# Kernel tuning notes

Hardware: AMD Instinct MI355X
Metric: run time of the kernel (lower is better)

## Reference

```python
import jax, jax.numpy as jnp
import numpy as np

N_NODES = 50000
N_EDGES = 800000
D_IN = 512
D_OUT = 256


def setup_inputs() -> dict:
    key = jax.random.key(0)
    k1, k2, k3 = jax.random.split(key, 3)
    x = jax.random.normal(k1, (N_NODES, D_IN), dtype=jnp.float32)
    edge_index = jax.random.randint(k2, (2, N_EDGES), 0, N_NODES, dtype=jnp.int64)
    # Glorot-style init for the GCN weight, zero bias (PyG defaults)
    W = jax.random.normal(k3, (D_IN, D_OUT), dtype=jnp.float32) * (1.0 / np.sqrt(D_IN))
    b = jnp.zeros((D_OUT,), dtype=jnp.float32)
    return {"x": x, "edge_index": edge_index, "W": W, "b": b}


def reference(x, edge_index, W, b):
    N = x.shape[0]
    # 1) dense linear transform (the compute-heavy GEMM)
    xw = x @ W  # [N, d_out]

    # 2) add self-loops (PyG GCNConv default)
    loop = jnp.arange(N, dtype=edge_index.dtype)
    row = jnp.concatenate([edge_index[0], loop])  # sources
    col = jnp.concatenate([edge_index[1], loop])  # targets

    # 3) symmetric normalization deg^{-1/2} on targets (in-degree incl. self-loops)
    deg = jax.ops.segment_sum(jnp.ones_like(col, dtype=xw.dtype), col, num_segments=N)
    dinv = jnp.where(deg > 0, jax.lax.rsqrt(deg), 0.0)
    norm = dinv[row] * dinv[col]  # [E+N]

    # 4) gather source features, scale, scatter-add to targets
    msgs = xw[row] * norm[:, None]  # [E+N, d_out]
    agg = jax.ops.segment_sum(msgs, col, num_segments=N)  # [N, d_out]

    # 5) bias + ReLU (dropout is identity in eval mode)
    return jax.nn.relu(agg + b)
```

## Files before the change

### kernel.cpp

```cpp
#include <hip/hip_runtime.h>
#include <hip/hip_bf16.h>

#define N_NODES 50000
#define N_EDGES 800000
#define D_IN    512
#define D_OUT   256
#define NBLK_SCAN ((N_NODES + 1023) / 1024)
#define GEMM_NWG (((N_NODES + 127) / 128) * 2)
#define GEMM_Q   (GEMM_NWG / 8)
#define GEMM_R   (GEMM_NWG % 8)

typedef short s8v  __attribute__((ext_vector_type(8)));
typedef float f32x4 __attribute__((ext_vector_type(4)));

__device__ __forceinline__ unsigned short bf16b(float f) {
    __hip_bfloat16 h = __float2bfloat16(f);
    return *reinterpret_cast<unsigned short*>(&h);
}
__device__ __forceinline__ float bflo(unsigned u) { return __uint_as_float(u << 16); }
__device__ __forceinline__ float bfhi(unsigned u) { return __uint_as_float(u & 0xffff0000u); }

#define GLD16(gp, lp)                                                           \
    __builtin_amdgcn_global_load_lds(                                           \
        (const __attribute__((address_space(1))) unsigned int*)(const void*)(gp),\
        (__attribute__((address_space(3))) unsigned int*)(void*)(lp), 16, 0, 0)

__device__ __forceinline__ int wave_incl_scan(int v, int lane) {
    #pragma unroll
    for (int d = 1; d < 64; d <<= 1) {
        int u = __shfl_up(v, d, 64);
        if (lane >= d) v += u;
    }
    return v;
}


__global__ void k_count(const int* __restrict__ col, int* __restrict__ cnt) {
    int i = (blockIdx.x * 256 + threadIdx.x) * 2;
    if (i < N_EDGES) {
        int2 c = *(const int2*)&col[i];
        atomicAdd(&cnt[c.x], 1);
        atomicAdd(&cnt[c.y], 1);
    }
}

__launch_bounds__(256)
__global__ void k_scan1(const int* __restrict__ cnt, int* __restrict__ bsum) {
    const int t = threadIdx.x, b = blockIdx.x;
    const int idx = b * 1024 + t * 4;
    int4 v = make_int4(0, 0, 0, 0);
    if (idx < N_NODES) v = *(const int4*)&cnt[idx];
    int s = v.x + v.y + v.z + v.w;
    #pragma unroll
    for (int d = 1; d < 64; d <<= 1) s += __shfl_xor(s, d, 64);
    __shared__ int ws[4];
    if ((t & 63) == 0) ws[t >> 6] = s;
    __syncthreads();
    if (t == 0) bsum[b] = ws[0] + ws[1] + ws[2] + ws[3];
}

__launch_bounds__(256)
__global__ void k_scan3(const int* __restrict__ cnt, const int* __restrict__ bsum,
                        int* __restrict__ row_ptr, float* __restrict__ dinv,
                        int* __restrict__ cursor) {
    const int t = threadIdx.x, b = blockIdx.x;
    const int lane = t & 63, wv = t >> 6;
    const int idx = b * 1024 + t * 4;
    int4 v = make_int4(0, 0, 0, 0);
    if (idx < N_NODES) v = *(const int4*)&cnt[idx];
    int s = v.x + v.y + v.z + v.w;
    int isc = wave_incl_scan(s, lane);
    __shared__ int wsum[4];
    __shared__ int s_boff;
    if (lane == 63) wsum[wv] = isc;
    if (t < 64) {
        int u = (t < b) ? bsum[t] : 0;
        #pragma unroll
        for (int d = 1; d < 64; d <<= 1) u += __shfl_xor(u, d, 64);
        if (t == 0) s_boff = u;
    }
    __syncthreads();
    int off = s_boff;
    #pragma unroll
    for (int i = 0; i < 4; ++i)
        if (i < wv) off += wsum[i];
    int p0 = off + isc - s;
    int p1 = p0 + v.x;
    int p2 = p1 + v.y;
    int p3 = p2 + v.z;
    if (idx < N_NODES) {
        row_ptr[idx + 0] = p0; cursor[idx + 0] = p0; dinv[idx + 0] = rsqrtf(1.f + (float)v.x);
        row_ptr[idx + 1] = p1; cursor[idx + 1] = p1; dinv[idx + 1] = rsqrtf(1.f + (float)v.y);
        row_ptr[idx + 2] = p2; cursor[idx + 2] = p2; dinv[idx + 2] = rsqrtf(1.f + (float)v.z);
        row_ptr[idx + 3] = p3; cursor[idx + 3] = p3; dinv[idx + 3] = rsqrtf(1.f + (float)v.w);
    }
    if (b == 0 && t == 0) row_ptr[N_NODES] = N_EDGES;
}

__global__ void k_fill(const int* __restrict__ row, const int* __restrict__ col,
                       int* __restrict__ cursor, int* __restrict__ csr_src) {
    int i = (blockIdx.x * 256 + threadIdx.x) * 2;
    if (i < N_EDGES) {
        int2 c = *(const int2*)&col[i];
        int2 r = *(const int2*)&row[i];
        int p0 = atomicAdd(&cursor[c.x], 1);
        csr_src[p0] = r.x;
        int p1 = atomicAdd(&cursor[c.y], 1);
        csr_src[p1] = r.y;
    }
}

__global__ void k_wt(const float* __restrict__ W, unsigned short* __restrict__ Wt) {
    int k = blockIdx.x;
    int n = threadIdx.x;
    Wt[(size_t)n * D_IN + k] = bf16b(W[(size_t)k * D_OUT + n]);
}

__launch_bounds__(256)
__global__ void k_gemm(const float* __restrict__ A,
                       const unsigned short* __restrict__ Wt,
                       const float* __restrict__ dinv,
                       unsigned short* __restrict__ yb)
{
    __shared__ __align__(16) float          As[128 * 32];
    __shared__ __align__(16) unsigned short Bs[128 * 32];

    int orig = blockIdx.x;
    int xcd = orig % 8, pos = orig / 8;
    int wg = (xcd < GEMM_R) ? xcd * (GEMM_Q + 1) + pos
                            : GEMM_R * (GEMM_Q + 1) + (xcd - GEMM_R) * GEMM_Q + pos;
    const int nt = wg & 1;
    const int mt = wg >> 1;
    const int m0 = mt * 128;
    const int n0 = nt * 128;

    const int t  = threadIdx.x;
    const int w  = t >> 6;
    const int l  = t & 63;
    const int wm = (w >> 1) * 64;
    const int wn = (w & 1) * 64;
    const int lr = l & 15;
    const int lk = l >> 4;

    size_t aoff[4];
    #pragma unroll
    for (int i = 0; i < 4; ++i) {
        int r = m0 + w * 32 + i * 8 + (l >> 3);
        if (r >= N_NODES) r = 0;
        aoff[i] = (size_t)r * D_IN + ((l & 7) ^ (l >> 3)) * 4;
    }
    size_t boff[2];
    #pragma unroll
    for (int i = 0; i < 2; ++i) {
        int r = n0 + w * 32 + i * 16 + (l >> 2);
        boff[i] = (size_t)r * D_IN + ((l & 3) ^ ((l >> 3) & 3)) * 8;
    }

    f32x4 acc[4][4] = {};

    #pragma unroll 1
    for (int tk = 0; tk < 16; ++tk) {
        const int kk = tk * 32;
        {
            char* ab = (char*)As + w * 4096;
            char* bb = (char*)Bs + w * 2048;
            #pragma unroll
            for (int i = 0; i < 4; ++i) GLD16(&A[aoff[i] + kk], ab + i * 1024);
            #pragma unroll
            for (int i = 0; i < 2; ++i) GLD16(&Wt[boff[i] + kk], bb + i * 1024);
        }
        __syncthreads();
        {
            s8v af[4], bfr[4];
            #pragma unroll
            for (int f = 0; f < 4; ++f) {
                int row = wm + f * 16 + lr;
                int s0  = (2 * lk) ^ (lr & 7);
                const char* pr = (const char*)As + row * 128;
                float4 x0 = *(const float4*)(pr + s0 * 16);
                float4 x1 = *(const float4*)(pr + (s0 ^ 1) * 16);
                union { s8v v; unsigned short h[8]; } u;
                u.h[0] = bf16b(x0.x); u.h[1] = bf16b(x0.y);
                u.h[2] = bf16b(x0.z); u.h[3] = bf16b(x0.w);
                u.h[4] = bf16b(x1.x); u.h[5] = bf16b(x1.y);
                u.h[6] = bf16b(x1.z); u.h[7] = bf16b(x1.w);
                af[f] = u.v;
            }
            #pragma unroll
            for (int f = 0; f < 4; ++f) {
                int row = wn + f * 16 + lr;
                int s   = lk ^ ((lr >> 1) & 3);
                bfr[f] = *(const s8v*)((const char*)Bs + row * 64 + s * 16);
            }
            #pragma unroll
            for (int fm = 0; fm < 4; ++fm)
                #pragma unroll
                for (int fn = 0; fn < 4; ++fn)
                    acc[fm][fn] = __builtin_amdgcn_mfma_f32_16x16x32_bf16(
                        af[fm], bfr[fn], acc[fm][fn], 0, 0, 0);
        }
        __syncthreads();
    }

    #pragma unroll
    for (int fm = 0; fm < 4; ++fm) {
        #pragma unroll
        for (int j = 0; j < 4; ++j) {
            int row = m0 + wm + fm * 16 + lk * 4 + j;
            if (row < N_NODES) {
                float s = dinv[row];
                #pragma unroll
                for (int fn = 0; fn < 4; ++fn) {
                    int col = n0 + wn + fn * 16 + lr;
                    yb[(size_t)row * D_OUT + col] = bf16b(acc[fm][fn][j] * s);
                }
            }
        }
    }
}

__device__ __forceinline__ void add8(float* acc, uint4 q) {
    unsigned x;
    x = q.x; acc[0] += bflo(x); acc[1] += bfhi(x);
    x = q.y; acc[2] += bflo(x); acc[3] += bfhi(x);
    x = q.z; acc[4] += bflo(x); acc[5] += bfhi(x);
    x = q.w; acc[6] += bflo(x); acc[7] += bfhi(x);
}

__launch_bounds__(256)
__global__ void k_gather(const int* __restrict__ row_ptr, const int* __restrict__ csr_src,
                         const unsigned short* __restrict__ yb, const float* __restrict__ dinv,
                         const float* __restrict__ bias, float* __restrict__ out)
{
    const int c  = blockIdx.x * 4 + (threadIdx.x >> 6);
    const int l  = threadIdx.x & 63;
    const int eg = l >> 5;
    const int cs = l & 31;
    const size_t colb = (size_t)cs * 8;

    float acc[8] = {0.f,0.f,0.f,0.f,0.f,0.f,0.f,0.f};

    const int s = row_ptr[c];
    const int e = row_ptr[c + 1];

    int i = s + eg;
    while (i + 14 < e) {
        int r[8];
        #pragma unroll
        for (int u = 0; u < 8; ++u) r[u] = csr_src[i + 2 * u];
        uint4 v[8];
        #pragma unroll
        for (int u = 0; u < 8; ++u) v[u] = *(const uint4*)&yb[(size_t)r[u] * D_OUT + colb];
        #pragma unroll
        for (int u = 0; u < 8; ++u) add8(acc, v[u]);
        i += 16;
    }
    while (i < e) {
        int r[4];
        #pragma unroll
        for (int u = 0; u < 4; ++u) {
            int p = i + 2 * u;
            r[u] = csr_src[p < e ? p : e - 1];
        }
        uint4 v[4];
        #pragma unroll
        for (int u = 0; u < 4; ++u) v[u] = *(const uint4*)&yb[(size_t)r[u] * D_OUT + colb];
        #pragma unroll
        for (int u = 0; u < 4; ++u)
            if (i + 2 * u < e) add8(acc, v[u]);
        i += 8;
    }

    #pragma unroll
    for (int u = 0; u < 8; ++u) acc[u] += __shfl_xor(acc[u], 32, 64);

    uint4 sv = *(const uint4*)&yb[(size_t)c * D_OUT + colb];
    add8(acc, sv);

    if (eg == 0) {
        const float sc = dinv[c];
        float4 b0 = *(const float4*)&bias[colb];
        float4 b1 = *(const float4*)&bias[colb + 4];
        float4 o0, o1;
        o0.x = fmaxf(fmaf(acc[0], sc, b0.x), 0.f);
        o0.y = fmaxf(fmaf(acc[1], sc, b0.y), 0.f);
        o0.z = fmaxf(fmaf(acc[2], sc, b0.z), 0.f);
        o0.w = fmaxf(fmaf(acc[3], sc, b0.w), 0.f);
        o1.x = fmaxf(fmaf(acc[4], sc, b1.x), 0.f);
        o1.y = fmaxf(fmaf(acc[5], sc, b1.y), 0.f);
        o1.z = fmaxf(fmaf(acc[6], sc, b1.z), 0.f);
        o1.w = fmaxf(fmaf(acc[7], sc, b1.w), 0.f);
        float* dst = &out[(size_t)c * D_OUT + colb];
        *(float4*)dst       = o0;
        *(float4*)(dst + 4) = o1;
    }
}

extern "C" void kernel_launch(void* const* d_in, const int* in_sizes, int n_in,
                              void* d_out, int out_size, void* d_ws, size_t ws_size,
                              hipStream_t stream) {
    const float* x   = (const float*)d_in[0];
    const int*   ei  = (const int*)d_in[1];
    const float* W   = (const float*)d_in[2];
    const float* b   = (const float*)d_in[3];
    float*       out = (float*)d_out;

    const int* row = ei;
    const int* col = ei + N_EDGES;

    char* p = (char*)d_ws;
    unsigned short* yb = (unsigned short*)p;  p += (size_t)N_NODES * D_OUT * 2;
    unsigned short* Wt = (unsigned short*)p;  p += (size_t)D_OUT * D_IN * 2;
    int*   csr_src = (int*)p;                 p += (size_t)N_EDGES * 4;
    int*   cnt     = (int*)p;                 p += (size_t)N_NODES * 4;
    int*   row_ptr = (int*)p;                 p += (size_t)(N_NODES + 4) * 4;
    int*   cursor  = (int*)p;                 p += (size_t)N_NODES * 4;
    float* dinv    = (float*)p;               p += (size_t)N_NODES * 4;
    int*   bsum    = (int*)p;                 p += (size_t)NBLK_SCAN * 4;

    hipMemsetAsync(cnt, 0, (size_t)N_NODES * sizeof(int), stream);
    k_count<<<(N_EDGES / 2 + 255) / 256, 256, 0, stream>>>(col, cnt);
    k_scan1<<<NBLK_SCAN, 256, 0, stream>>>(cnt, bsum);
    k_scan3<<<NBLK_SCAN, 256, 0, stream>>>(cnt, bsum, row_ptr, dinv, cursor);
    k_fill <<<(N_EDGES / 2 + 255) / 256, 256, 0, stream>>>(row, col, cursor, csr_src);
    k_wt   <<<D_IN, D_OUT, 0, stream>>>(W, Wt);

    k_gemm<<<GEMM_NWG, 256, 0, stream>>>(x, Wt, dinv, yb);

    k_gather<<<N_NODES / 4, 256, 0, stream>>>(row_ptr, csr_src, yb, dinv, b, out);
}
```

Before: 209.2 us.

## Split degree counters into four replicas, fuse memset into Wt kernel, deepen GEMM K-tile

```diff
diff --git a/kernel.cpp b/kernel.cpp
--- a/kernel.cpp
+++ b/kernel.cpp
@@ -34,23 +34,40 @@
     return v;
 }
 
-
-__global__ void k_count(const int* __restrict__ col, int* __restrict__ cnt) {
+__global__ void k_wt(const float* __restrict__ W, unsigned short* __restrict__ Wt,
+                     int* __restrict__ cnt4) {
+    int k = blockIdx.x;
+    int n = threadIdx.x;
+    Wt[(size_t)n * D_IN + k] = bf16b(W[(size_t)k * D_OUT + n]);
+    int t = (blockIdx.x * 256 + threadIdx.x) * 2;
+    if (t < 4 * N_NODES) {
+        cnt4[t] = 0;
+        if (t + 1 < 4 * N_NODES) cnt4[t + 1] = 0;
+    }
+}
+
+
+__global__ void k_count(const int* __restrict__ col, int* __restrict__ cnt4) {
     int i = (blockIdx.x * 256 + threadIdx.x) * 2;
     if (i < N_EDGES) {
         int2 c = *(const int2*)&col[i];
-        atomicAdd(&cnt[c.x], 1);
-        atomicAdd(&cnt[c.y], 1);
+        atomicAdd(&cnt4[(i & 3) * N_NODES + c.x], 1);
+        atomicAdd(&cnt4[((i + 1) & 3) * N_NODES + c.y], 1);
     }
 }
 
 __launch_bounds__(256)
-__global__ void k_scan1(const int* __restrict__ cnt, int* __restrict__ bsum) {
+__global__ void k_scan1(const int* __restrict__ cnt4, int* __restrict__ bsum) {
     const int t = threadIdx.x, b = blockIdx.x;
     const int idx = b * 1024 + t * 4;
-    int4 v = make_int4(0, 0, 0, 0);
-    if (idx < N_NODES) v = *(const int4*)&cnt[idx];
-    int s = v.x + v.y + v.z + v.w;
+    int s = 0;
+    if (idx < N_NODES) {
+        #pragma unroll
+        for (int q = 0; q < 4; ++q) {
+            int4 v = *(const int4*)&cnt4[q * N_NODES + idx];
+            s += (v.x + v.y) + (v.z + v.w);
+        }
+    }
     #pragma unroll
     for (int d = 1; d < 64; d <<= 1) s += __shfl_xor(s, d, 64);
     __shared__ int ws[4];
@@ -60,15 +77,26 @@
 }
 
 __launch_bounds__(256)
-__global__ void k_scan3(const int* __restrict__ cnt, const int* __restrict__ bsum,
+__global__ void k_scan3(const int* __restrict__ cnt4, const int* __restrict__ bsum,
                         int* __restrict__ row_ptr, float* __restrict__ dinv,
-                        int* __restrict__ cursor) {
+                        int* __restrict__ cursor4) {
     const int t = threadIdx.x, b = blockIdx.x;
     const int lane = t & 63, wv = t >> 6;
     const int idx = b * 1024 + t * 4;
-    int4 v = make_int4(0, 0, 0, 0);
-    if (idx < N_NODES) v = *(const int4*)&cnt[idx];
-    int s = v.x + v.y + v.z + v.w;
+    int4 vq[4];
+    int4 tot = make_int4(0, 0, 0, 0);
+    if (idx < N_NODES) {
+        #pragma unroll
+        for (int q = 0; q < 4; ++q) {
+            vq[q] = *(const int4*)&cnt4[q * N_NODES + idx];
+            tot.x += vq[q].x; tot.y += vq[q].y;
+            tot.z += vq[q].z; tot.w += vq[q].w;
+        }
+    } else {
+        #pragma unroll
+        for (int q = 0; q < 4; ++q) vq[q] = make_int4(0, 0, 0, 0);
+    }
+    int s = (tot.x + tot.y) + (tot.z + tot.w);
     int isc = wave_incl_scan(s, lane);
     __shared__ int wsum[4];
     __shared__ int s_boff;
@@ -85,35 +113,36 @@
     for (int i = 0; i < 4; ++i)
         if (i < wv) off += wsum[i];
     int p0 = off + isc - s;
-    int p1 = p0 + v.x;
-    int p2 = p1 + v.y;
-    int p3 = p2 + v.z;
+    int p1 = p0 + tot.x;
+    int p2 = p1 + tot.y;
+    int p3 = p2 + tot.z;
     if (idx < N_NODES) {
-        row_ptr[idx + 0] = p0; cursor[idx + 0] = p0; dinv[idx + 0] = rsqrtf(1.f + (float)v.x);
-        row_ptr[idx + 1] = p1; cursor[idx + 1] = p1; dinv[idx + 1] = rsqrtf(1.f + (float)v.y);
-        row_ptr[idx + 2] = p2; cursor[idx + 2] = p2; dinv[idx + 2] = rsqrtf(1.f + (float)v.z);
-        row_ptr[idx + 3] = p3; cursor[idx + 3] = p3; dinv[idx + 3] = rsqrtf(1.f + (float)v.w);
+        row_ptr[idx + 0] = p0; dinv[idx + 0] = rsqrtf(1.f + (float)tot.x);
+        row_ptr[idx + 1] = p1; dinv[idx + 1] = rsqrtf(1.f + (float)tot.y);
+        row_ptr[idx + 2] = p2; dinv[idx + 2] = rsqrtf(1.f + (float)tot.z);
+        row_ptr[idx + 3] = p3; dinv[idx + 3] = rsqrtf(1.f + (float)tot.w);
+        int4 run = make_int4(p0, p1, p2, p3);
+        #pragma unroll
+        for (int q = 0; q < 4; ++q) {
+            *(int4*)&cursor4[q * N_NODES + idx] = run;
+            run.x += vq[q].x; run.y += vq[q].y;
+            run.z += vq[q].z; run.w += vq[q].w;
+        }
     }
     if (b == 0 && t == 0) row_ptr[N_NODES] = N_EDGES;
 }
 
 __global__ void k_fill(const int* __restrict__ row, const int* __restrict__ col,
-                       int* __restrict__ cursor, int* __restrict__ csr_src) {
+                       int* __restrict__ cursor4, int* __restrict__ csr_src) {
     int i = (blockIdx.x * 256 + threadIdx.x) * 2;
     if (i < N_EDGES) {
         int2 c = *(const int2*)&col[i];
         int2 r = *(const int2*)&row[i];
-        int p0 = atomicAdd(&cursor[c.x], 1);
+        int p0 = atomicAdd(&cursor4[(i & 3) * N_NODES + c.x], 1);
         csr_src[p0] = r.x;
-        int p1 = atomicAdd(&cursor[c.y], 1);
+        int p1 = atomicAdd(&cursor4[((i + 1) & 3) * N_NODES + c.y], 1);
         csr_src[p1] = r.y;
     }
-}
-
-__global__ void k_wt(const float* __restrict__ W, unsigned short* __restrict__ Wt) {
-    int k = blockIdx.x;
-    int n = threadIdx.x;
-    Wt[(size_t)n * D_IN + k] = bf16b(W[(size_t)k * D_OUT + n]);
 }
 
 __launch_bounds__(256)
@@ -122,8 +151,8 @@
                        const float* __restrict__ dinv,
                        unsigned short* __restrict__ yb)
 {
-    __shared__ __align__(16) float          As[128 * 32];
-    __shared__ __align__(16) unsigned short Bs[128 * 32];
+    __shared__ __align__(16) float          As[128 * 64];
+    __shared__ __align__(16) unsigned short Bs[128 * 64];
 
     int orig = blockIdx.x;
     int xcd = orig % 8, pos = orig / 8;
@@ -142,43 +171,47 @@
     const int lr = l & 15;
     const int lk = l >> 4;
 
-    size_t aoff[4];
+    size_t aoff[8];
+    #pragma unroll
+    for (int i = 0; i < 8; ++i) {
+        int row = m0 + w * 32 + i * 4 + (l >> 4);
+        if (row >= N_NODES) row = 0;
+        int sslot = (l & 15) ^ (row & 7);
+        aoff[i] = (size_t)row * D_IN + sslot * 4;
+    }
+    const int srow = l >> 3;
+    const int srcj = (l & 7) ^ srow;
+    size_t boff[4];
     #pragma unroll
     for (int i = 0; i < 4; ++i) {
-        int r = m0 + w * 32 + i * 8 + (l >> 3);
-        if (r >= N_NODES) r = 0;
-        aoff[i] = (size_t)r * D_IN + ((l & 7) ^ (l >> 3)) * 4;
-    }
-    size_t boff[2];
-    #pragma unroll
-    for (int i = 0; i < 2; ++i) {
-        int r = n0 + w * 32 + i * 16 + (l >> 2);
-        boff[i] = (size_t)r * D_IN + ((l & 3) ^ ((l >> 3) & 3)) * 8;
+        int g = w * 4 + i;
+        int bn = n0 + g * 8 + srow;
+        boff[i] = (size_t)bn * D_IN + srcj * 8;
     }
 
     f32x4 acc[4][4] = {};
 
-    #pragma unroll 1
-    for (int tk = 0; tk < 16; ++tk) {
-        const int kk = tk * 32;
-        {
-            char* ab = (char*)As + w * 4096;
-            char* bb = (char*)Bs + w * 2048;
-            #pragma unroll
-            for (int i = 0; i < 4; ++i) GLD16(&A[aoff[i] + kk], ab + i * 1024);
-            #pragma unroll
-            for (int i = 0; i < 2; ++i) GLD16(&Wt[boff[i] + kk], bb + i * 1024);
-        }
+    for (int kk = 0; kk < D_IN; kk += 64) {
+        #pragma unroll
+        for (int i = 0; i < 8; ++i)
+            GLD16(&A[aoff[i] + kk], (char*)As + (w * 32 + i * 4) * 256);
+        #pragma unroll
+        for (int i = 0; i < 4; ++i)
+            GLD16(&Wt[boff[i] + kk], (char*)Bs + (w * 4 + i) * 1024);
         __syncthreads();
-        {
+
+        #pragma unroll
+        for (int ks = 0; ks < 2; ++ks) {
             s8v af[4], bfr[4];
             #pragma unroll
             for (int f = 0; f < 4; ++f) {
                 int row = wm + f * 16 + lr;
-                int s0  = (2 * lk) ^ (lr & 7);
-                const char* pr = (const char*)As + row * 128;
+                int a   = (ks * 4 + lk) * 2;
+                int s0  = a ^ (lr & 7);
+                int s1  = (a + 1) ^ (lr & 7);
+                const char* pr = (const char*)As + row * 256;
                 float4 x0 = *(const float4*)(pr + s0 * 16);
-                float4 x1 = *(const float4*)(pr + (s0 ^ 1) * 16);
+                float4 x1 = *(const float4*)(pr + s1 * 16);
                 union { s8v v; unsigned short h[8]; } u;
                 u.h[0] = bf16b(x0.x); u.h[1] = bf16b(x0.y);
                 u.h[2] = bf16b(x0.z); u.h[3] = bf16b(x0.w);
@@ -186,12 +219,10 @@
                 u.h[6] = bf16b(x1.z); u.h[7] = bf16b(x1.w);
                 af[f] = u.v;
             }
+            const int kb = (ks * 64 + lk * 16) ^ ((lr & 7) << 4);
             #pragma unroll
-            for (int f = 0; f < 4; ++f) {
-                int row = wn + f * 16 + lr;
-                int s   = lk ^ ((lr >> 1) & 3);
-                bfr[f] = *(const s8v*)((const char*)Bs + row * 64 + s * 16);
-            }
+            for (int f = 0; f < 4; ++f)
+                bfr[f] = *(const s8v*)((const char*)Bs + ((wn + f * 16 + lr) * 128 + kb));
             #pragma unroll
             for (int fm = 0; fm < 4; ++fm)
                 #pragma unroll
@@ -312,18 +343,17 @@
     unsigned short* yb = (unsigned short*)p;  p += (size_t)N_NODES * D_OUT * 2;
     unsigned short* Wt = (unsigned short*)p;  p += (size_t)D_OUT * D_IN * 2;
     int*   csr_src = (int*)p;                 p += (size_t)N_EDGES * 4;
-    int*   cnt     = (int*)p;                 p += (size_t)N_NODES * 4;
+    int*   cnt4    = (int*)p;                 p += (size_t)4 * N_NODES * 4;
     int*   row_ptr = (int*)p;                 p += (size_t)(N_NODES + 4) * 4;
-    int*   cursor  = (int*)p;                 p += (size_t)N_NODES * 4;
+    int*   cursor4 = (int*)p;                 p += (size_t)4 * N_NODES * 4;
     float* dinv    = (float*)p;               p += (size_t)N_NODES * 4;
     int*   bsum    = (int*)p;                 p += (size_t)NBLK_SCAN * 4;
 
-    hipMemsetAsync(cnt, 0, (size_t)N_NODES * sizeof(int), stream);
-    k_count<<<(N_EDGES / 2 + 255) / 256, 256, 0, stream>>>(col, cnt);
-    k_scan1<<<NBLK_SCAN, 256, 0, stream>>>(cnt, bsum);
-    k_scan3<<<NBLK_SCAN, 256, 0, stream>>>(cnt, bsum, row_ptr, dinv, cursor);
-    k_fill <<<(N_EDGES / 2 + 255) / 256, 256, 0, stream>>>(row, col, cursor, csr_src);
-    k_wt   <<<D_IN, D_OUT, 0, stream>>>(W, Wt);
+    k_wt   <<<D_IN, D_OUT, 0, stream>>>(W, Wt, cnt4);
+    k_count<<<(N_EDGES / 2 + 255) / 256, 256, 0, stream>>>(col, cnt4);
+    k_scan1<<<NBLK_SCAN, 256, 0, stream>>>(cnt4, bsum);
+    k_scan3<<<NBLK_SCAN, 256, 0, stream>>>(cnt4, bsum, row_ptr, dinv, cursor4);
+    k_fill <<<(N_EDGES / 2 + 255) / 256, 256, 0, stream>>>(row, col, cursor4, csr_src);
 
     k_gemm<<<GEMM_NWG, 256, 0, stream>>>(x, Wt, dinv, yb);
 
```

Measured after the change: 193.5 us. 7.5% less time.
